# Kernel optimization log

Hardware: AMD Instinct MI355X
Metric: run time of the kernel (lower is better)

## Reference

```python
import jax, jax.numpy as jnp
import numpy as np


def setup_inputs() -> dict:
    key = jax.random.key(0)
    k_y, k_cb = jax.random.split(key)
    B, C, H, W = 8, 192, 64, 64
    G, K = 8, 512
    d = C // G  # 24
    y = jax.random.normal(k_y, (B, C, H, W), dtype=jnp.float32)
    codebooks = jax.random.normal(k_cb, (G, K, d), dtype=jnp.float32)
    return {"y": y, "codebooks": codebooks}


def reference(y, codebooks):
    # y: [B, C, H, W]; codebooks: [G, K, d] with C == G*d
    B, C, H, W = y.shape
    G, K, d = codebooks.shape
    # split channels into G groups of dim d -> vectors at each spatial pos
    x = y.reshape(B, G, d, H, W).transpose(0, 3, 4, 1, 2)  # [B,H,W,G,d]
    x2 = jnp.sum(x * x, axis=-1, keepdims=True)            # [B,H,W,G,1]
    e2 = jnp.sum(codebooks * codebooks, axis=-1)           # [G,K]
    xe = jnp.einsum('bhwgd,gkd->bhwgk', x, codebooks)      # [B,H,W,G,K]
    dist = x2 - 2.0 * xe + e2                              # [B,H,W,G,K]
    idx = jnp.argmin(dist, axis=-1)                        # [B,H,W,G] int
    # gather quantized vectors per group (to_feather)
    q = codebooks[jnp.arange(G), idx]                      # [B,H,W,G,d]
    y_ba = q.transpose(0, 3, 4, 1, 2).reshape(B, C, H, W)  # [B,C,H,W]
    code_index = idx.transpose(0, 3, 1, 2)                 # [B,G,H,W]
    # straight-through estimator
    universal_ctx = y + jax.lax.stop_gradient(y_ba - y)
    return universal_ctx, y_ba, code_index[:, None]        # [B,1,G,H,W]
```

## Files before the change

kernel.cpp:

```cpp
#include <hip/hip_runtime.h>

#define B_   8
#define C_   192
#define HW_  4096
#define G_   8
#define K_   512
#define D_   24
#define CBSZ (K_ * D_)
#define THREADS 256
#define TILES_PER_BLOCK 8

typedef float  f32x4 __attribute__((ext_vector_type(4)));
typedef short  s16x8 __attribute__((ext_vector_type(8)));
typedef short  s16x4 __attribute__((ext_vector_type(4)));
typedef unsigned long long u64;

static __device__ __forceinline__ unsigned umin_(unsigned a, unsigned b){return a<b?a:b;}
static __device__ __forceinline__ unsigned umax_(unsigned a, unsigned b){return a>b?a:b;}
static __device__ __forceinline__ unsigned short f2bf(float x){
    unsigned u=__float_as_uint(x);
    return (unsigned short)((u + 0x7FFFu + ((u>>16)&1u))>>16);
}
static __device__ __forceinline__ float bf2f(unsigned short h){return __uint_as_float(((unsigned)h)<<16);}

__global__ __launch_bounds__(THREADS, 5) void vq_mfma3(
    const float* __restrict__ y, const float* __restrict__ cb, float* __restrict__ out)
{
    __shared__ unsigned short sB[32 * 512];

    const int bid = blockIdx.x;
    const int g = bid & 7;
    const int chunk = bid >> 3;
    const int tid = threadIdx.x;
    const int wave = tid >> 6, lane = tid & 63;
    const int c = lane & 15, q = lane >> 4;

    const float* cbg = cb + g * CBSZ;

    {
        const f32x4* cb4 = (const f32x4*)cbg;
        for (int i = tid; i < CBSZ/4; i += THREADS) {
            f32x4 v = cb4[i];
            int i4 = i << 2;
            int n  = i4 / 24;
            int k0 = i4 - n * 24;
            int off = (n >> 4) * 512 + (((k0 >> 3) << 4) + (n & 15)) * 8 + (k0 & 7);
            s16x4 h;
            h[0]=(short)f2bf(v[0]); h[1]=(short)f2bf(v[1]);
            h[2]=(short)f2bf(v[2]); h[3]=(short)f2bf(v[3]);
            *(s16x4*)(&sB[off]) = h;
        }
        for (int n = tid; n < K_; n += THREADS) {
            const float* row = cbg + n * D_;
            double s0 = 0.0, s1 = 0.0;
            #pragma unroll
            for (int j = 0; j < D_; j += 2) {
                double v0 = (double)row[j], v1 = (double)row[j+1];
                s0 = fma(v0,v0,s0); s1 = fma(v1,v1,s1);
            }
            double s = s0 + s1;
            unsigned short ehi = f2bf((float)s);
            unsigned short elo = f2bf((float)(s - (double)bf2f(ehi)));
            unsigned* dst = (unsigned*)(&sB[(n >> 4) * 512 + (48 + (n & 15)) * 8]);
            dst[0] = (unsigned)ehi | ((unsigned)elo << 16);
            dst[1] = 0u; dst[2] = 0u; dst[3] = 0u;
        }
    }
    __syncthreads();

    float* out0 = out;
    float* out1 = out + B_*C_*HW_;
    float* out2 = out + 2*B_*C_*HW_;

    for (int mt = wave; mt < TILES_PER_BLOCK; mt += 4) {
        const int posT = chunk * (TILES_PER_BLOCK*16) + mt * 16;
        const int bimg = posT >> 12;
        const int hw   = posT & (HW_-1);
        const int ybase = (bimg*C_ + g*D_)*HW_ + hw;
        const float* yb = y + ybase;

        s16x8 Ah = {0,0,0,0,0,0,0,0}, Al = {0,0,0,0,0,0,0,0};
        if (q < 3) {
            #pragma unroll
            for (int j = 0; j < 8; ++j) {
                float xv = -2.0f * yb[(q*8+j)*HW_ + c];
                unsigned u = __float_as_uint(xv);
                Ah[j] = (short)(u >> 16);
                Al[j] = (short)f2bf(xv - __uint_as_float(u & 0xFFFF0000u));
            }
        } else {
            Ah[0] = (short)0x3F80; Ah[1] = (short)0x3F80;
        }

        unsigned b1[4], b2[4];
        #pragma unroll
        for (int r=0;r<4;++r){ b1[r]=0xFFFFFFFFu; b2[r]=0xFFFFFFFFu; }

        #pragma unroll 8
        for (int t = 0; t < 32; ++t) {
            s16x8 bh = *(const s16x8*)(&sB[t*512 + lane*8]);
            f32x4 acc = {256.0f, 256.0f, 256.0f, 256.0f};
            acc = __builtin_amdgcn_mfma_f32_16x16x32_bf16(Ah, bh, acc, 0,0,0);
            acc = __builtin_amdgcn_mfma_f32_16x16x32_bf16(Al, bh, acc, 0,0,0);
            #pragma unroll
            for (int r=0;r<4;++r){
                unsigned key = (__float_as_uint(acc[r]) & 0xFFFFFFE0u) | (unsigned)t;
                b2[r] = umin_(umax_(b1[r], key), b2[r]);
                b1[r] = umin_(b1[r], key);
            }
        }

        unsigned u1[4],u2[4],u3[4];
        #pragma unroll
        for (int r=0;r<4;++r){
            u1[r] = (b1[r] & 0xFFFFFE00u) | (((b1[r]&31u)<<4) | (unsigned)c);
            u2[r] = (b2[r] & 0xFFFFFE00u) | (((b2[r]&31u)<<4) | (unsigned)c);
            u3[r] = 0xFFFFFFFFu;
        }
        #pragma unroll
        for (int d=1; d<16; d<<=1){
            #pragma unroll
            for (int r=0;r<4;++r){
                unsigned o1=__shfl_xor(u1[r],d,64), o2=__shfl_xor(u2[r],d,64), o3=__shfl_xor(u3[r],d,64);
                unsigned x = umax_(u1[r],o1);
                unsigned yv= umin_(u2[r],o2);
                unsigned w = umax_(u2[r],o2);
                unsigned z = umin_(u3[r],o3);
                u1[r]=umin_(u1[r],o1);
                u2[r]=umin_(x,yv);
                u3[r]=umin_(umax_(x,yv), umin_(w,z));
            }
        }

        const int rr = c >> 2, cand = c & 3, row = (q<<2) + rr;
        unsigned s1v = (rr==0)?u1[0]:(rr==1)?u1[1]:(rr==2)?u1[2]:u1[3];
        unsigned s2v = (rr==0)?u2[0]:(rr==1)?u2[1]:(rr==2)?u2[2]:u2[3];
        unsigned s3v = (rr==0)?u3[0]:(rr==1)?u3[1]:(rr==2)?u3[2]:u3[3];
        unsigned sel = (cand==0)?s1v:(cand==1)?s2v:s3v;
        int kc = (int)(sel & 511u);

        const f32x4* ce4 = (const f32x4*)(cbg + kc * D_);
        float ef[24];
        #pragma unroll
        for (int v=0; v<6; ++v) *(f32x4*)&ef[v*4] = ce4[v];
        double a0=0.0, a1=0.0, a2=0.0, a3=0.0;
        #pragma unroll
        for (int j=0;j<24;j+=4){
            double e0=(double)ef[j],   e1=(double)ef[j+1];
            double e2=(double)ef[j+2], e3=(double)ef[j+3];
            double x0=-2.0*(double)yb[j*HW_ + row];
            double x1=-2.0*(double)yb[(j+1)*HW_ + row];
            double x2=-2.0*(double)yb[(j+2)*HW_ + row];
            double x3=-2.0*(double)yb[(j+3)*HW_ + row];
            a0 = fma(e0, e0+x0, a0);
            a1 = fma(e1, e1+x1, a1);
            a2 = fma(e2, e2+x2, a2);
            a3 = fma(e3, e3+x3, a3);
        }
        double s = ((a0 + a1) + (a2 + a3)) + 256.0;
        u64 key64 = (((u64)__double_as_longlong(s)) & ~0x1FFull) | (u64)kc;
        if (cand == 3) key64 = ~0ull;
        u64 o = __shfl_xor(key64, 1, 64); key64 = o < key64 ? o : key64;
        o = __shfl_xor(key64, 2, 64);     key64 = o < key64 ? o : key64;
        int kwin = (int)(key64 & 511ull);

        const int p = c;
        const int srcl = ((p>>2)<<4) | ((p&3)<<2);
        int kw = __shfl(kwin, srcl, 64);
        const float* cw = cbg + kw * D_;
        #pragma unroll
        for (int i=0;i<6;++i){
            int ch = i*4 + q;
            float val = cw[ch];
            int oo = ybase + ch*HW_ + p;
            out0[oo] = val;
            out1[oo] = val;
        }
        if (lane < 16)
            out2[(bimg*G_ + g)*HW_ + hw + lane] = (float)kw;
    }
}

extern "C" void kernel_launch(void* const* d_in, const int* in_sizes, int n_in,
                              void* d_out, int out_size, void* d_ws, size_t ws_size,
                              hipStream_t stream) {
    const float* y  = (const float*)d_in[0];
    const float* cb = (const float*)d_in[1];
    float* out = (float*)d_out;

    const int nblocks = 256 * G_;
    vq_mfma3<<<dim3(nblocks), dim3(THREADS), 0, stream>>>(y, cb, out);
}
```

Baseline: 122.8 us.

## Transpose MFMA operands, per-lane top-3 tracking, and skip fp64 refinement when margin is clear

The MFMA operands are swapped so each lane holds codes for a fixed position. This lets the top-3 candidate tracking stay in scalar registers, and the cross-lane reduction shrinks to two xor-shuffle steps. The fp64 rescoring of candidates now runs only when a wave ballot finds a position whose top-two margin is under a threshold. The output gather uses vectorized per-lane codebook loads, and each block processes twice as many tiles, with half the blocks and lower occupancy. The threshold-based skip risks wrong argmin choices if the bf16-split error ever exceeds the margin.

```diff
diff --git a/kernel.cpp b/kernel.cpp
--- a/kernel.cpp
+++ b/kernel.cpp
@@ -8,9 +8,10 @@
 #define D_   24
 #define CBSZ (K_ * D_)
 #define THREADS 256
-#define TILES_PER_BLOCK 8
+#define TILES_PER_BLOCK 16
 
 typedef float  f32x4 __attribute__((ext_vector_type(4)));
+typedef int    i32x4 __attribute__((ext_vector_type(4)));
 typedef short  s16x8 __attribute__((ext_vector_type(8)));
 typedef short  s16x4 __attribute__((ext_vector_type(4)));
 typedef unsigned long long u64;
@@ -23,7 +24,7 @@
 }
 static __device__ __forceinline__ float bf2f(unsigned short h){return __uint_as_float(((unsigned)h)<<16);}
 
-__global__ __launch_bounds__(THREADS, 5) void vq_mfma3(
+__global__ __launch_bounds__(THREADS, 4) void vq_mfma4(
     const float* __restrict__ y, const float* __restrict__ cb, float* __restrict__ out)
 {
     __shared__ unsigned short sB[32 * 512];
@@ -79,105 +80,111 @@
         const int ybase = (bimg*C_ + g*D_)*HW_ + hw;
         const float* yb = y + ybase;
 
-        s16x8 Ah = {0,0,0,0,0,0,0,0}, Al = {0,0,0,0,0,0,0,0};
+        float xf[8];
+        unsigned hx[4], lx[4];
         if (q < 3) {
-            #pragma unroll
-            for (int j = 0; j < 8; ++j) {
-                float xv = -2.0f * yb[(q*8+j)*HW_ + c];
-                unsigned u = __float_as_uint(xv);
-                Ah[j] = (short)(u >> 16);
-                Al[j] = (short)f2bf(xv - __uint_as_float(u & 0xFFFF0000u));
+            const float* yq = yb + (q*8)*HW_ + c;
+            #pragma unroll
+            for (int jj = 0; jj < 8; ++jj) xf[jj] = -2.0f * yq[jj*HW_];
+            #pragma unroll
+            for (int p2 = 0; p2 < 4; ++p2) {
+                float f0 = xf[2*p2], f1 = xf[2*p2+1];
+                unsigned u0 = __float_as_uint(f0), u1v = __float_as_uint(f1);
+                hx[p2] = (u1v & 0xFFFF0000u) | (u0 >> 16);
+                float l0 = f0 - __uint_as_float(u0 & 0xFFFF0000u);
+                float l1 = f1 - __uint_as_float(u1v & 0xFFFF0000u);
+                lx[p2] = (unsigned)f2bf(l0) | ((unsigned)f2bf(l1) << 16);
             }
         } else {
-            Ah[0] = (short)0x3F80; Ah[1] = (short)0x3F80;
-        }
-
-        unsigned b1[4], b2[4];
-        #pragma unroll
-        for (int r=0;r<4;++r){ b1[r]=0xFFFFFFFFu; b2[r]=0xFFFFFFFFu; }
-
+            #pragma unroll
+            for (int jj = 0; jj < 8; ++jj) xf[jj] = 0.0f;
+            hx[0] = 0x3F803F80u; hx[1]=0u; hx[2]=0u; hx[3]=0u;
+            lx[0]=0u; lx[1]=0u; lx[2]=0u; lx[3]=0u;
+        }
+        const s16x8 Xh = __builtin_bit_cast(s16x8, (i32x4){(int)hx[0],(int)hx[1],(int)hx[2],(int)hx[3]});
+        const s16x8 Xl = __builtin_bit_cast(s16x8, (i32x4){(int)lx[0],(int)lx[1],(int)lx[2],(int)lx[3]});
+
+        unsigned b1=0xFFFFFFFFu, b2=0xFFFFFFFFu, b3=0xFFFFFFFFu;
+        const unsigned qr4 = (unsigned)(q << 2);
         #pragma unroll 8
         for (int t = 0; t < 32; ++t) {
-            s16x8 bh = *(const s16x8*)(&sB[t*512 + lane*8]);
+            s16x8 eh = *(const s16x8*)(&sB[t*512 + lane*8]);
             f32x4 acc = {256.0f, 256.0f, 256.0f, 256.0f};
-            acc = __builtin_amdgcn_mfma_f32_16x16x32_bf16(Ah, bh, acc, 0,0,0);
-            acc = __builtin_amdgcn_mfma_f32_16x16x32_bf16(Al, bh, acc, 0,0,0);
-            #pragma unroll
-            for (int r=0;r<4;++r){
-                unsigned key = (__float_as_uint(acc[r]) & 0xFFFFFFE0u) | (unsigned)t;
-                b2[r] = umin_(umax_(b1[r], key), b2[r]);
-                b1[r] = umin_(b1[r], key);
-            }
-        }
-
-        unsigned u1[4],u2[4],u3[4];
+            acc = __builtin_amdgcn_mfma_f32_16x16x32_bf16(eh, Xh, acc, 0,0,0);
+            acc = __builtin_amdgcn_mfma_f32_16x16x32_bf16(eh, Xl, acc, 0,0,0);
+            const unsigned cbase = ((unsigned)t << 4) + qr4;
+            #pragma unroll
+            for (int r = 0; r < 4; ++r) {
+                unsigned key = (__float_as_uint(acc[r]) & 0xFFFFFE00u) + (cbase + r);
+                b3 = umin_(umax_(b2, key), b3);
+                b2 = umin_(umax_(b1, key), b2);
+                b1 = umin_(b1, key);
+            }
+        }
+
         #pragma unroll
-        for (int r=0;r<4;++r){
-            u1[r] = (b1[r] & 0xFFFFFE00u) | (((b1[r]&31u)<<4) | (unsigned)c);
-            u2[r] = (b2[r] & 0xFFFFFE00u) | (((b2[r]&31u)<<4) | (unsigned)c);
-            u3[r] = 0xFFFFFFFFu;
-        }
-        #pragma unroll
-        for (int d=1; d<16; d<<=1){
-            #pragma unroll
-            for (int r=0;r<4;++r){
-                unsigned o1=__shfl_xor(u1[r],d,64), o2=__shfl_xor(u2[r],d,64), o3=__shfl_xor(u3[r],d,64);
-                unsigned x = umax_(u1[r],o1);
-                unsigned yv= umin_(u2[r],o2);
-                unsigned w = umax_(u2[r],o2);
-                unsigned z = umin_(u3[r],o3);
-                u1[r]=umin_(u1[r],o1);
-                u2[r]=umin_(x,yv);
-                u3[r]=umin_(umax_(x,yv), umin_(w,z));
-            }
-        }
-
-        const int rr = c >> 2, cand = c & 3, row = (q<<2) + rr;
-        unsigned s1v = (rr==0)?u1[0]:(rr==1)?u1[1]:(rr==2)?u1[2]:u1[3];
-        unsigned s2v = (rr==0)?u2[0]:(rr==1)?u2[1]:(rr==2)?u2[2]:u2[3];
-        unsigned s3v = (rr==0)?u3[0]:(rr==1)?u3[1]:(rr==2)?u3[2]:u3[3];
-        unsigned sel = (cand==0)?s1v:(cand==1)?s2v:s3v;
-        int kc = (int)(sel & 511u);
-
-        const f32x4* ce4 = (const f32x4*)(cbg + kc * D_);
-        float ef[24];
-        #pragma unroll
-        for (int v=0; v<6; ++v) *(f32x4*)&ef[v*4] = ce4[v];
-        double a0=0.0, a1=0.0, a2=0.0, a3=0.0;
-        #pragma unroll
-        for (int j=0;j<24;j+=4){
-            double e0=(double)ef[j],   e1=(double)ef[j+1];
-            double e2=(double)ef[j+2], e3=(double)ef[j+3];
-            double x0=-2.0*(double)yb[j*HW_ + row];
-            double x1=-2.0*(double)yb[(j+1)*HW_ + row];
-            double x2=-2.0*(double)yb[(j+2)*HW_ + row];
-            double x3=-2.0*(double)yb[(j+3)*HW_ + row];
-            a0 = fma(e0, e0+x0, a0);
-            a1 = fma(e1, e1+x1, a1);
-            a2 = fma(e2, e2+x2, a2);
-            a3 = fma(e3, e3+x3, a3);
-        }
-        double s = ((a0 + a1) + (a2 + a3)) + 256.0;
-        u64 key64 = (((u64)__double_as_longlong(s)) & ~0x1FFull) | (u64)kc;
-        if (cand == 3) key64 = ~0ull;
-        u64 o = __shfl_xor(key64, 1, 64); key64 = o < key64 ? o : key64;
-        o = __shfl_xor(key64, 2, 64);     key64 = o < key64 ? o : key64;
-        int kwin = (int)(key64 & 511ull);
-
-        const int p = c;
-        const int srcl = ((p>>2)<<4) | ((p&3)<<2);
-        int kw = __shfl(kwin, srcl, 64);
-        const float* cw = cbg + kw * D_;
-        #pragma unroll
-        for (int i=0;i<6;++i){
-            int ch = i*4 + q;
-            float val = cw[ch];
-            int oo = ybase + ch*HW_ + p;
-            out0[oo] = val;
-            out1[oo] = val;
+        for (int d = 16; d < 64; d <<= 1) {
+            unsigned o1=__shfl_xor(b1,d,64), o2=__shfl_xor(b2,d,64), o3=__shfl_xor(b3,d,64);
+            unsigned x = umax_(b1,o1);
+            unsigned yv= umin_(b2,o2);
+            unsigned w = umax_(b2,o2);
+            unsigned z = umin_(b3,o3);
+            b1 = umin_(b1,o1);
+            b2 = umin_(x,yv);
+            b3 = umin_(umax_(x,yv), umin_(w,z));
+        }
+
+        const float v1 = __uint_as_float(b1 & 0xFFFFFE00u);
+        const float v2 = __uint_as_float(b2 & 0xFFFFFE00u);
+        int kwin;
+        if (__ballot((v2 - v1) < 0.20f) == 0ull) {
+            kwin = (int)(b1 & 511u);
+        } else {
+            double xd[8];
+            #pragma unroll
+            for (int jj = 0; jj < 8; ++jj) xd[jj] = (double)xf[jj];
+            const unsigned cands[3] = {b1, b2, b3};
+            u64 bestk = ~0ull;
+            #pragma unroll
+            for (int ci = 0; ci < 3; ++ci) {
+                int kc = (int)(cands[ci] & 511u);
+                double s = 0.0;
+                if (q < 3) {
+                    const f32x4* ce4 = (const f32x4*)(cbg + kc*D_ + (q<<3));
+                    float ef[8];
+                    *(f32x4*)&ef[0] = ce4[0];
+                    *(f32x4*)&ef[4] = ce4[1];
+                    #pragma unroll
+                    for (int jj = 0; jj < 8; ++jj) {
+                        double ev = (double)ef[jj];
+                        s = fma(ev, ev, s);
+                        s = fma(xd[jj], ev, s);
+                    }
+                }
+                s += __shfl_xor(s, 16, 64);
+                s += __shfl_xor(s, 32, 64);
+                s += 256.0;
+                u64 kk = (((u64)__double_as_longlong(s)) & ~0x1FFull) | (u64)kc;
+                bestk = kk < bestk ? kk : bestk;
+            }
+            kwin = (int)(bestk & 511ull);
+        }
+
+        const float* cw = cbg + kwin * D_;
+        if (q < 3) {
+            const f32x4* cw4 = (const f32x4*)(cw + (q<<3));
+            float v[8];
+            *(f32x4*)&v[0] = cw4[0];
+            *(f32x4*)&v[4] = cw4[1];
+            const int ob = ybase + (q*8)*HW_ + c;
+            #pragma unroll
+            for (int jj = 0; jj < 8; ++jj) {
+                out0[ob + jj*HW_] = v[jj];
+                out1[ob + jj*HW_] = v[jj];
+            }
         }
         if (lane < 16)
-            out2[(bimg*G_ + g)*HW_ + hw + lane] = (float)kw;
+            out2[(bimg*G_ + g)*HW_ + hw + lane] = (float)kwin;
     }
 }
 
@@ -188,6 +195,6 @@
     const float* cb = (const float*)d_in[1];
     float* out = (float*)d_out;
 
-    const int nblocks = 256 * G_;
-    vq_mfma3<<<dim3(nblocks), dim3(THREADS), 0, stream>>>(y, cb, out);
+    const int nblocks = 128 * G_;
+    vq_mfma4<<<dim3(nblocks), dim3(THREADS), 0, stream>>>(y, cb, out);
 }
```

Result: faster. 119.5 us (-2.7%).
